# Performance work log

Hardware: AMD Instinct MI355X
Metric: run time of the kernel (lower is better)

Reference implementation:

```python
import jax, jax.numpy as jnp
import numpy as np

CON_SIZE = 1024  # num_gz; used in the 1/sqrt(con_size) score scaling


def setup_inputs() -> dict:
    key = jax.random.key(0)
    k1, k2, k3, k4, k5 = jax.random.split(key, 5)
    B, K, D, P = 1024, 256, 1024, 768
    return {
        "joint_feature": jax.random.normal(k1, (B, D), dtype=jnp.float32),
        "confounder_dictionary": jax.random.normal(k2, (K, D), dtype=jnp.float32),
        "prior": jax.random.uniform(k3, (K, 1), dtype=jnp.float32),
        "Wq": jax.random.normal(k4, (D, P), dtype=jnp.float32) * (1.0 / np.sqrt(D)),
        "Wk": jax.random.normal(k5, (D, P), dtype=jnp.float32) * (1.0 / np.sqrt(D)),
    }


def reference(joint_feature, confounder_dictionary, prior, Wq, Wk):
    # dot_product_intervention
    q = joint_feature @ Wq                       # [B, 768]
    k = confounder_dictionary @ Wk               # [K, 768]
    scores = (q @ k.T) * (1.0 / jnp.sqrt(jnp.float32(CON_SIZE)))  # [B, K]
    attn = jax.nn.softmax(scores, axis=-1)       # softmax over confounders
    # (attn[b,k,1] * conf[k,d] * prior[k,1]).sum(1)  == attn @ (conf * prior)
    g_z = jnp.einsum('bk,kd->bd', attn, confounder_dictionary * prior)  # [B, D]
    return joint_feature + g_z
```

## Files before the change

### kernel.cpp

```cpp
#include <hip/hip_runtime.h>
#include <hip/hip_bf16.h>


typedef __attribute__((ext_vector_type(8))) short short8;
typedef __attribute__((ext_vector_type(4))) float f32x4;

__device__ __forceinline__ ushort f2bf(float x) {
    union { float f; uint u; } c; c.f = x;
    return (ushort)((c.u + 0x7FFFu + ((c.u >> 16) & 1u)) >> 16);
}
__device__ __forceinline__ float bflo(uint u) {
    union { uint u; float f; } c; c.u = u << 16; return c.f;
}
__device__ __forceinline__ float bfhi(uint u) {
    union { uint u; float f; } c; c.u = u & 0xFFFF0000u; return c.f;
}

#define MFMA_BF16 __builtin_amdgcn_mfma_f32_16x16x32_bf16

__global__ __launch_bounds__(256)
void prep_kernel(const float* __restrict__ J, const float* __restrict__ conf,
                 const float* __restrict__ prior, const float* __restrict__ Wq,
                 const float* __restrict__ Wk,
                 ushort* __restrict__ Jb, ushort* __restrict__ confb,
                 ushort* __restrict__ Wqb, ushort* __restrict__ Wkb,
                 ushort* __restrict__ cpT)
{
    const int t = threadIdx.x;
    int b = blockIdx.x;

    if (b < 2816) {
        const float* src; ushort* dst; int base;
        if (b < 1024)      { src = J;    dst = Jb;    base = b * 1024; }
        else if (b < 1280) { src = conf; dst = confb; base = (b - 1024) * 1024; }
        else if (b < 2048) { src = Wq;   dst = Wqb;   base = (b - 1280) * 1024; }
        else               { src = Wk;   dst = Wkb;   base = (b - 2048) * 1024; }
        const float4 v = *(const float4*)(src + base + t * 4);
        ushort4 o;
        o.x = f2bf(v.x); o.y = f2bf(v.y); o.z = f2bf(v.z); o.w = f2bf(v.w);
        *(ushort4*)(dst + base + t * 4) = o;
        return;
    }

    __shared__ float tr[32][33];
    const int b2 = b - 2816;
    const int rt = b2 >> 5, ct = b2 & 31;
    {
        const int row = t >> 3, c4 = (t & 7) << 2;
        const float4 v = *(const float4*)(conf + (size_t)(rt * 32 + row) * 1024 + ct * 32 + c4);
        const float p = prior[rt * 32 + row];
        tr[row][c4 + 0] = v.x * p; tr[row][c4 + 1] = v.y * p;
        tr[row][c4 + 2] = v.z * p; tr[row][c4 + 3] = v.w * p;
    }
    __syncthreads();
    {
        const int orow = t >> 3, oc4 = (t & 7) << 2;
        ushort4 o;
        o.x = f2bf(tr[oc4 + 0][orow]); o.y = f2bf(tr[oc4 + 1][orow]);
        o.z = f2bf(tr[oc4 + 2][orow]); o.w = f2bf(tr[oc4 + 3][orow]);
        *(ushort4*)(cpT + (size_t)(ct * 32 + orow) * 256 + rt * 32 + oc4) = o;
    }
}

__global__ __launch_bounds__(256)
void qk_kernel(const ushort* __restrict__ Jb, const ushort* __restrict__ Wqb,
               const ushort* __restrict__ confb, const ushort* __restrict__ Wkb,
               ushort* __restrict__ qb, ushort* __restrict__ kmb)
{
    __shared__ __align__(16) ushort As[64][72];
    __shared__ __align__(16) ushort Bs[64][72];

    const int t = threadIdx.x;
    int bid = blockIdx.x;
    const ushort *A, *Wb; ushort* C;
    if (bid < 192) { A = Jb; Wb = Wqb; C = qb; }
    else           { bid -= 192; A = confb; Wb = Wkb; C = kmb; }
    const int m0 = (bid / 12) * 64, n0 = (bid % 12) * 64;

    const int wave = t >> 6, lane = t & 63;
    const int wm = (wave >> 1) * 32, wn = (wave & 1) * 32;
    const int lrow = lane & 15, quad = lane >> 4, lko = quad * 8;

    f32x4 acc[2][2];
    #pragma unroll
    for (int i = 0; i < 2; ++i)
        #pragma unroll
        for (int j = 0; j < 2; ++j) acc[i][j] = (f32x4)0.0f;

    const int sr = t >> 2, sk = (t & 3) << 4;
    const ushort* Ap = A + (size_t)(m0 + sr) * 1024 + sk;
    const int bn8 = (t & 7) * 8, bkp = t >> 3;
    const ushort* Bp = Wb + (size_t)(2 * bkp) * 768 + n0 + bn8;

    uint4 av0 = *(const uint4*)(Ap);
    uint4 av1 = *(const uint4*)(Ap + 8);
    uint4 b0  = *(const uint4*)(Bp);
    uint4 b1  = *(const uint4*)(Bp + 768);

    for (int k0 = 0; k0 < 1024; k0 += 64) {
        *(uint4*)&As[sr][sk]     = av0;
        *(uint4*)&As[sr][sk + 8] = av1;
        {
            const ushort* s0 = (const ushort*)&b0;
            const ushort* s1 = (const ushort*)&b1;
            #pragma unroll
            for (int i = 0; i < 8; ++i)
                *(uint*)&Bs[bn8 + i][2 * bkp] = (uint)s0[i] | ((uint)s1[i] << 16);
        }
        __syncthreads();
        if (k0 + 64 < 1024) {
            av0 = *(const uint4*)(Ap + k0 + 64);
            av1 = *(const uint4*)(Ap + k0 + 72);
            const ushort* Bn = Bp + (size_t)(k0 + 64) * 768;
            b0 = *(const uint4*)(Bn);
            b1 = *(const uint4*)(Bn + 768);
        }
        #pragma unroll
        for (int kk = 0; kk < 64; kk += 32) {
            const short8 a0 = *(const short8*)&As[wm + lrow][kk + lko];
            const short8 a1 = *(const short8*)&As[wm + 16 + lrow][kk + lko];
            const short8 bb0 = *(const short8*)&Bs[wn + lrow][kk + lko];
            const short8 bb1 = *(const short8*)&Bs[wn + 16 + lrow][kk + lko];
            acc[0][0] = MFMA_BF16(a0, bb0, acc[0][0], 0, 0, 0);
            acc[0][1] = MFMA_BF16(a0, bb1, acc[0][1], 0, 0, 0);
            acc[1][0] = MFMA_BF16(a1, bb0, acc[1][0], 0, 0, 0);
            acc[1][1] = MFMA_BF16(a1, bb1, acc[1][1], 0, 0, 0);
        }
        __syncthreads();
    }

    #pragma unroll
    for (int i = 0; i < 2; ++i)
        #pragma unroll
        for (int j = 0; j < 2; ++j)
            #pragma unroll
            for (int r = 0; r < 4; ++r) {
                const int m = m0 + wm + i * 16 + quad * 4 + r;
                const int n = n0 + wn + j * 16 + lrow;
                C[(size_t)m * 768 + n] = f2bf(acc[i][j][r]);
            }
}

__global__ __launch_bounds__(256)
void scores_kernel(const ushort* __restrict__ qb, const ushort* __restrict__ kmb,
                   ushort* __restrict__ sc)
{
    __shared__ __align__(16) ushort As[64][72];
    __shared__ __align__(16) ushort Bs[64][72];

    const int t = threadIdx.x;
    const int m0 = blockIdx.y * 64, n0 = blockIdx.x * 64;
    const int wave = t >> 6, lane = t & 63;
    const int wm = (wave >> 1) * 32, wn = (wave & 1) * 32;
    const int lrow = lane & 15, quad = lane >> 4, lko = quad * 8;

    f32x4 acc[2][2];
    #pragma unroll
    for (int i = 0; i < 2; ++i)
        #pragma unroll
        for (int j = 0; j < 2; ++j) acc[i][j] = (f32x4)0.0f;

    const int sr = t >> 2, sk = (t & 3) << 4;
    const ushort* Ap = qb  + (size_t)(m0 + sr) * 768 + sk;
    const ushort* Bp = kmb + (size_t)(n0 + sr) * 768 + sk;

    uint4 av0 = *(const uint4*)(Ap);
    uint4 av1 = *(const uint4*)(Ap + 8);
    uint4 bv0 = *(const uint4*)(Bp);
    uint4 bv1 = *(const uint4*)(Bp + 8);

    for (int k0 = 0; k0 < 768; k0 += 64) {
        *(uint4*)&As[sr][sk]     = av0;
        *(uint4*)&As[sr][sk + 8] = av1;
        *(uint4*)&Bs[sr][sk]     = bv0;
        *(uint4*)&Bs[sr][sk + 8] = bv1;
        __syncthreads();
        if (k0 + 64 < 768) {
            av0 = *(const uint4*)(Ap + k0 + 64);
            av1 = *(const uint4*)(Ap + k0 + 72);
            bv0 = *(const uint4*)(Bp + k0 + 64);
            bv1 = *(const uint4*)(Bp + k0 + 72);
        }
        #pragma unroll
        for (int kk = 0; kk < 64; kk += 32) {
            const short8 a0 = *(const short8*)&As[wm + lrow][kk + lko];
            const short8 a1 = *(const short8*)&As[wm + 16 + lrow][kk + lko];
            const short8 b0 = *(const short8*)&Bs[wn + lrow][kk + lko];
            const short8 b1 = *(const short8*)&Bs[wn + 16 + lrow][kk + lko];
            acc[0][0] = MFMA_BF16(a0, b0, acc[0][0], 0, 0, 0);
            acc[0][1] = MFMA_BF16(a0, b1, acc[0][1], 0, 0, 0);
            acc[1][0] = MFMA_BF16(a1, b0, acc[1][0], 0, 0, 0);
            acc[1][1] = MFMA_BF16(a1, b1, acc[1][1], 0, 0, 0);
        }
        __syncthreads();
    }

    #pragma unroll
    for (int i = 0; i < 2; ++i)
        #pragma unroll
        for (int j = 0; j < 2; ++j)
            #pragma unroll
            for (int r = 0; r < 4; ++r) {
                const int m = m0 + wm + i * 16 + quad * 4 + r;
                const int n = n0 + wn + j * 16 + lrow;
                sc[(size_t)m * 256 + n] = f2bf(acc[i][j][r] * 0.03125f);
            }
}

__global__ __launch_bounds__(256)
void out_kernel(const ushort* __restrict__ sc, const ushort* __restrict__ cpT,
                const float* __restrict__ J, float* __restrict__ out)
{
    __shared__ __align__(16) ushort At[64][264];
    __shared__ __align__(16) ushort Bs[64][72];
    __shared__ float rowInv[64];

    const int t = threadIdx.x;
    const int m0 = blockIdx.y * 64, n0 = blockIdx.x * 64;

    {
        const int row = t >> 2;
        const int cb  = (t & 3) * 64;
        const ushort* srow = sc + (size_t)(m0 + row) * 256 + cb;
        uint4 s[8];
        #pragma unroll
        for (int i = 0; i < 8; ++i) s[i] = *(const uint4*)(srow + i * 8);

        float mx = -1e30f;
        #pragma unroll
        for (int i = 0; i < 8; ++i) {
            mx = fmaxf(mx, fmaxf(fmaxf(bflo(s[i].x), bfhi(s[i].x)),
                                 fmaxf(bflo(s[i].y), bfhi(s[i].y))));
            mx = fmaxf(mx, fmaxf(fmaxf(bflo(s[i].z), bfhi(s[i].z)),
                                 fmaxf(bflo(s[i].w), bfhi(s[i].w))));
        }
        mx = fmaxf(mx, __shfl_xor(mx, 1));
        mx = fmaxf(mx, __shfl_xor(mx, 2));

        float sum = 0.0f;
        #pragma unroll
        for (int i = 0; i < 8; ++i) {
            uint4 o;
            uint* su = (uint*)&s[i];
            uint* ou = (uint*)&o;
            #pragma unroll
            for (int w = 0; w < 4; ++w) {
                const ushort e0 = f2bf(__expf(bflo(su[w]) - mx));
                const ushort e1 = f2bf(__expf(bfhi(su[w]) - mx));
                sum += bflo((uint)e0) + bflo((uint)e1);
                ou[w] = (uint)e0 | ((uint)e1 << 16);
            }
            *(uint4*)&At[row][cb + i * 8] = o;
        }
        sum += __shfl_xor(sum, 1);
        sum += __shfl_xor(sum, 2);
        if ((t & 3) == 0) rowInv[row] = 1.0f / sum;
    }
    __syncthreads();

    const int wave = t >> 6, lane = t & 63;
    const int wm = (wave >> 1) * 32, wn = (wave & 1) * 32;
    const int lrow = lane & 15, quad = lane >> 4, lko = quad * 8;

    f32x4 acc[2][2];
    #pragma unroll
    for (int i = 0; i < 2; ++i)
        #pragma unroll
        for (int j = 0; j < 2; ++j) acc[i][j] = (f32x4)0.0f;

    const int sr = t >> 2, sk = (t & 3) << 4;
    const ushort* Bp = cpT + (size_t)(n0 + sr) * 256 + sk;
    uint4 bv0 = *(const uint4*)(Bp);
    uint4 bv1 = *(const uint4*)(Bp + 8);

    for (int k0 = 0; k0 < 256; k0 += 64) {
        *(uint4*)&Bs[sr][sk]     = bv0;
        *(uint4*)&Bs[sr][sk + 8] = bv1;
        __syncthreads();
        if (k0 + 64 < 256) {
            bv0 = *(const uint4*)(Bp + k0 + 64);
            bv1 = *(const uint4*)(Bp + k0 + 72);
        }
        #pragma unroll
        for (int kk = 0; kk < 64; kk += 32) {
            const short8 a0 = *(const short8*)&At[wm + lrow][k0 + kk + lko];
            const short8 a1 = *(const short8*)&At[wm + 16 + lrow][k0 + kk + lko];
            const short8 b0 = *(const short8*)&Bs[wn + lrow][kk + lko];
            const short8 b1 = *(const short8*)&Bs[wn + 16 + lrow][kk + lko];
            acc[0][0] = MFMA_BF16(a0, b0, acc[0][0], 0, 0, 0);
            acc[0][1] = MFMA_BF16(a0, b1, acc[0][1], 0, 0, 0);
            acc[1][0] = MFMA_BF16(a1, b0, acc[1][0], 0, 0, 0);
            acc[1][1] = MFMA_BF16(a1, b1, acc[1][1], 0, 0, 0);
        }
        __syncthreads();
    }

    #pragma unroll
    for (int i = 0; i < 2; ++i)
        #pragma unroll
        for (int j = 0; j < 2; ++j)
            #pragma unroll
            for (int r = 0; r < 4; ++r) {
                const int mrel = wm + i * 16 + quad * 4 + r;
                const int m = m0 + mrel;
                const int n = n0 + wn + j * 16 + lrow;
                const size_t off = (size_t)m * 1024 + n;
                out[off] = acc[i][j][r] * rowInv[mrel] + J[off];
            }
}

extern "C" void kernel_launch(void* const* d_in, const int* in_sizes, int n_in,
                              void* d_out, int out_size, void* d_ws, size_t ws_size,
                              hipStream_t stream)
{
    const float* J     = (const float*)d_in[0];
    const float* conf  = (const float*)d_in[1];
    const float* prior = (const float*)d_in[2];
    const float* Wq    = (const float*)d_in[3];
    const float* Wk    = (const float*)d_in[4];
    float* out = (float*)d_out;

    ushort* ws = (ushort*)d_ws;
    ushort* Jb    = ws;
    ushort* confb = Jb    + 1048576;
    ushort* Wqb   = confb + 262144;
    ushort* Wkb   = Wqb   + 786432;
    ushort* cpT   = Wkb   + 786432;
    ushort* qb    = cpT   + 262144;
    ushort* kmb   = qb    + 786432;
    ushort* scb   = kmb   + 196608;

    prep_kernel<<<3072, 256, 0, stream>>>(J, conf, prior, Wq, Wk,
                                          Jb, confb, Wqb, Wkb, cpT);
    qk_kernel<<<240, 256, 0, stream>>>(Jb, Wqb, confb, Wkb, qb, kmb);
    scores_kernel<<<dim3(4, 16), 256, 0, stream>>>(qb, kmb, scb);
    out_kernel<<<dim3(16, 16), 256, 0, stream>>>(scb, cpT, J, out);
}
```

Measured before the change: 96.97 us.

## Fuse fp32-to-bf16 conversion into the Q/K projection GEMM and drop prep kernel

```diff
diff --git a/kernel.cpp b/kernel.cpp
--- a/kernel.cpp
+++ b/kernel.cpp
@@ -15,67 +15,58 @@
 __device__ __forceinline__ float bfhi(uint u) {
     union { uint u; float f; } c; c.u = u & 0xFFFF0000u; return c.f;
 }
+__device__ __forceinline__ uint fbits(float x) {
+    union { float f; uint u; } c; c.f = x; return c.u;
+}
+__device__ __forceinline__ uint pk_rhu(float lo, float hi) {
+    return ((fbits(lo) + 0x8000u) >> 16) | ((fbits(hi) + 0x8000u) & 0xFFFF0000u);
+}
 
 #define MFMA_BF16 __builtin_amdgcn_mfma_f32_16x16x32_bf16
 
+union Lds1 {
+    float tr[32][33];
+    struct {
+        __align__(16) ushort As[64][72];
+        __align__(16) ushort Bs[64][72];
+    } g;
+};
+
 __global__ __launch_bounds__(256)
-void prep_kernel(const float* __restrict__ J, const float* __restrict__ conf,
-                 const float* __restrict__ prior, const float* __restrict__ Wq,
-                 const float* __restrict__ Wk,
-                 ushort* __restrict__ Jb, ushort* __restrict__ confb,
-                 ushort* __restrict__ Wqb, ushort* __restrict__ Wkb,
-                 ushort* __restrict__ cpT)
+void l1_kernel(const float* __restrict__ J, const float* __restrict__ conf,
+               const float* __restrict__ prior, const float* __restrict__ Wq,
+               const float* __restrict__ Wk, ushort* __restrict__ qb,
+               ushort* __restrict__ kmb, ushort* __restrict__ cpT)
 {
+    __shared__ Lds1 S;
     const int t = threadIdx.x;
-    int b = blockIdx.x;
-
-    if (b < 2816) {
-        const float* src; ushort* dst; int base;
-        if (b < 1024)      { src = J;    dst = Jb;    base = b * 1024; }
-        else if (b < 1280) { src = conf; dst = confb; base = (b - 1024) * 1024; }
-        else if (b < 2048) { src = Wq;   dst = Wqb;   base = (b - 1280) * 1024; }
-        else               { src = Wk;   dst = Wkb;   base = (b - 2048) * 1024; }
-        const float4 v = *(const float4*)(src + base + t * 4);
-        ushort4 o;
-        o.x = f2bf(v.x); o.y = f2bf(v.y); o.z = f2bf(v.z); o.w = f2bf(v.w);
-        *(ushort4*)(dst + base + t * 4) = o;
+    const int bid = blockIdx.x;
+
+    if (bid >= 240) {
+        const int b2 = bid - 240;
+        const int rt = b2 >> 5, ct = b2 & 31;
+        {
+            const int row = t >> 3, c4 = (t & 7) << 2;
+            const float4 v = *(const float4*)(conf + (size_t)(rt * 32 + row) * 1024 + ct * 32 + c4);
+            const float p = prior[rt * 32 + row];
+            S.tr[row][c4 + 0] = v.x * p; S.tr[row][c4 + 1] = v.y * p;
+            S.tr[row][c4 + 2] = v.z * p; S.tr[row][c4 + 3] = v.w * p;
+        }
+        __syncthreads();
+        {
+            const int orow = t >> 3, oc4 = (t & 7) << 2;
+            ushort4 o;
+            o.x = f2bf(S.tr[oc4 + 0][orow]); o.y = f2bf(S.tr[oc4 + 1][orow]);
+            o.z = f2bf(S.tr[oc4 + 2][orow]); o.w = f2bf(S.tr[oc4 + 3][orow]);
+            *(ushort4*)(cpT + (size_t)(ct * 32 + orow) * 256 + rt * 32 + oc4) = o;
+        }
         return;
     }
 
-    __shared__ float tr[32][33];
-    const int b2 = b - 2816;
-    const int rt = b2 >> 5, ct = b2 & 31;
-    {
-        const int row = t >> 3, c4 = (t & 7) << 2;
-        const float4 v = *(const float4*)(conf + (size_t)(rt * 32 + row) * 1024 + ct * 32 + c4);
-        const float p = prior[rt * 32 + row];
-        tr[row][c4 + 0] = v.x * p; tr[row][c4 + 1] = v.y * p;
-        tr[row][c4 + 2] = v.z * p; tr[row][c4 + 3] = v.w * p;
-    }
-    __syncthreads();
-    {
-        const int orow = t >> 3, oc4 = (t & 7) << 2;
-        ushort4 o;
-        o.x = f2bf(tr[oc4 + 0][orow]); o.y = f2bf(tr[oc4 + 1][orow]);
-        o.z = f2bf(tr[oc4 + 2][orow]); o.w = f2bf(tr[oc4 + 3][orow]);
-        *(ushort4*)(cpT + (size_t)(ct * 32 + orow) * 256 + rt * 32 + oc4) = o;
-    }
-}
-
-__global__ __launch_bounds__(256)
-void qk_kernel(const ushort* __restrict__ Jb, const ushort* __restrict__ Wqb,
-               const ushort* __restrict__ confb, const ushort* __restrict__ Wkb,
-               ushort* __restrict__ qb, ushort* __restrict__ kmb)
-{
-    __shared__ __align__(16) ushort As[64][72];
-    __shared__ __align__(16) ushort Bs[64][72];
-
-    const int t = threadIdx.x;
-    int bid = blockIdx.x;
-    const ushort *A, *Wb; ushort* C;
-    if (bid < 192) { A = Jb; Wb = Wqb; C = qb; }
-    else           { bid -= 192; A = confb; Wb = Wkb; C = kmb; }
-    const int m0 = (bid / 12) * 64, n0 = (bid % 12) * 64;
+    const float *A, *Bm; ushort* C; int m0, n0;
+    if (bid < 192) { A = J;    Bm = Wq; C = qb;  m0 = (bid / 12) * 64; n0 = (bid % 12) * 64; }
+    else { const int b2 = bid - 192;
+           A = conf; Bm = Wk; C = kmb; m0 = (b2  / 12) * 64; n0 = (b2  % 12) * 64; }
 
     const int wave = t >> 6, lane = t & 63;
     const int wm = (wave >> 1) * 32, wn = (wave & 1) * 32;
@@ -87,44 +78,60 @@
         #pragma unroll
         for (int j = 0; j < 2; ++j) acc[i][j] = (f32x4)0.0f;
 
-    const int sr = t >> 2, sk = (t & 3) << 4;
-    const ushort* Ap = A + (size_t)(m0 + sr) * 1024 + sk;
-    const int bn8 = (t & 7) * 8, bkp = t >> 3;
-    const ushort* Bp = Wb + (size_t)(2 * bkp) * 768 + n0 + bn8;
-
-    uint4 av0 = *(const uint4*)(Ap);
-    uint4 av1 = *(const uint4*)(Ap + 8);
-    uint4 b0  = *(const uint4*)(Bp);
-    uint4 b1  = *(const uint4*)(Bp + 768);
+    const int sr = t >> 2, q4 = (t & 3) << 4;
+    const int bn = (t & 15) << 2, bk = (t >> 4) << 1;
+    const float* Ap = A + (size_t)(m0 + sr) * 1024 + q4;
+    const float* Bp = Bm + (size_t)bk * 768 + n0 + bn;
+
+    float4 aF0 = *(const float4*)(Ap + 0),  aF1 = *(const float4*)(Ap + 4);
+    float4 aF2 = *(const float4*)(Ap + 8),  aF3 = *(const float4*)(Ap + 12);
+    float4 bF0 = *(const float4*)(Bp);
+    float4 bF1 = *(const float4*)(Bp + 768);
+    float4 bF2 = *(const float4*)(Bp + (size_t)32 * 768);
+    float4 bF3 = *(const float4*)(Bp + (size_t)33 * 768);
 
     for (int k0 = 0; k0 < 1024; k0 += 64) {
-        *(uint4*)&As[sr][sk]     = av0;
-        *(uint4*)&As[sr][sk + 8] = av1;
         {
-            const ushort* s0 = (const ushort*)&b0;
-            const ushort* s1 = (const ushort*)&b1;
-            #pragma unroll
-            for (int i = 0; i < 8; ++i)
-                *(uint*)&Bs[bn8 + i][2 * bkp] = (uint)s0[i] | ((uint)s1[i] << 16);
+            uint2 w;
+            w.x = pk_rhu(aF0.x, aF0.y); w.y = pk_rhu(aF0.z, aF0.w);
+            *(uint2*)&S.g.As[sr][q4 + 0] = w;
+            w.x = pk_rhu(aF1.x, aF1.y); w.y = pk_rhu(aF1.z, aF1.w);
+            *(uint2*)&S.g.As[sr][q4 + 4] = w;
+            w.x = pk_rhu(aF2.x, aF2.y); w.y = pk_rhu(aF2.z, aF2.w);
+            *(uint2*)&S.g.As[sr][q4 + 8] = w;
+            w.x = pk_rhu(aF3.x, aF3.y); w.y = pk_rhu(aF3.z, aF3.w);
+            *(uint2*)&S.g.As[sr][q4 + 12] = w;
+            *(uint*)&S.g.Bs[bn + 0][bk]      = pk_rhu(bF0.x, bF1.x);
+            *(uint*)&S.g.Bs[bn + 1][bk]      = pk_rhu(bF0.y, bF1.y);
+            *(uint*)&S.g.Bs[bn + 2][bk]      = pk_rhu(bF0.z, bF1.z);
+            *(uint*)&S.g.Bs[bn + 3][bk]      = pk_rhu(bF0.w, bF1.w);
+            *(uint*)&S.g.Bs[bn + 0][bk + 32] = pk_rhu(bF2.x, bF3.x);
+            *(uint*)&S.g.Bs[bn + 1][bk + 32] = pk_rhu(bF2.y, bF3.y);
+            *(uint*)&S.g.Bs[bn + 2][bk + 32] = pk_rhu(bF2.z, bF3.z);
+            *(uint*)&S.g.Bs[bn + 3][bk + 32] = pk_rhu(bF2.w, bF3.w);
         }
         __syncthreads();
         if (k0 + 64 < 1024) {
-            av0 = *(const uint4*)(Ap + k0 + 64);
-            av1 = *(const uint4*)(Ap + k0 + 72);
-            const ushort* Bn = Bp + (size_t)(k0 + 64) * 768;
-            b0 = *(const uint4*)(Bn);
-            b1 = *(const uint4*)(Bn + 768);
+            aF0 = *(const float4*)(Ap + k0 + 64);
+            aF1 = *(const float4*)(Ap + k0 + 68);
+            aF2 = *(const float4*)(Ap + k0 + 72);
+            aF3 = *(const float4*)(Ap + k0 + 76);
+            const float* Bn = Bp + (size_t)(k0 + 64) * 768;
+            bF0 = *(const float4*)(Bn);
+            bF1 = *(const float4*)(Bn + 768);
+            bF2 = *(const float4*)(Bn + (size_t)32 * 768);
+            bF3 = *(const float4*)(Bn + (size_t)33 * 768);
         }
         #pragma unroll
         for (int kk = 0; kk < 64; kk += 32) {
-            const short8 a0 = *(const short8*)&As[wm + lrow][kk + lko];
-            const short8 a1 = *(const short8*)&As[wm + 16 + lrow][kk + lko];
-            const short8 bb0 = *(const short8*)&Bs[wn + lrow][kk + lko];
-            const short8 bb1 = *(const short8*)&Bs[wn + 16 + lrow][kk + lko];
-            acc[0][0] = MFMA_BF16(a0, bb0, acc[0][0], 0, 0, 0);
-            acc[0][1] = MFMA_BF16(a0, bb1, acc[0][1], 0, 0, 0);
-            acc[1][0] = MFMA_BF16(a1, bb0, acc[1][0], 0, 0, 0);
-            acc[1][1] = MFMA_BF16(a1, bb1, acc[1][1], 0, 0, 0);
+            const short8 a0 = *(const short8*)&S.g.As[wm + lrow][kk + lko];
+            const short8 a1 = *(const short8*)&S.g.As[wm + 16 + lrow][kk + lko];
+            const short8 b0 = *(const short8*)&S.g.Bs[wn + lrow][kk + lko];
+            const short8 b1 = *(const short8*)&S.g.Bs[wn + 16 + lrow][kk + lko];
+            acc[0][0] = MFMA_BF16(a0, b0, acc[0][0], 0, 0, 0);
+            acc[0][1] = MFMA_BF16(a0, b1, acc[0][1], 0, 0, 0);
+            acc[1][0] = MFMA_BF16(a1, b0, acc[1][0], 0, 0, 0);
+            acc[1][1] = MFMA_BF16(a1, b1, acc[1][1], 0, 0, 0);
         }
         __syncthreads();
     }
@@ -320,19 +327,13 @@
     const float* Wk    = (const float*)d_in[4];
     float* out = (float*)d_out;
 
-    ushort* ws = (ushort*)d_ws;
-    ushort* Jb    = ws;
-    ushort* confb = Jb    + 1048576;
-    ushort* Wqb   = confb + 262144;
-    ushort* Wkb   = Wqb   + 786432;
-    ushort* cpT   = Wkb   + 786432;
-    ushort* qb    = cpT   + 262144;
-    ushort* kmb   = qb    + 786432;
-    ushort* scb   = kmb   + 196608;
-
-    prep_kernel<<<3072, 256, 0, stream>>>(J, conf, prior, Wq, Wk,
-                                          Jb, confb, Wqb, Wkb, cpT);
-    qk_kernel<<<240, 256, 0, stream>>>(Jb, Wqb, confb, Wkb, qb, kmb);
+    ushort* ws  = (ushort*)d_ws;
+    ushort* qb  = ws;
+    ushort* kmb = qb  + 786432;
+    ushort* cpT = kmb + 196608;
+    ushort* scb = cpT + 262144;
+
+    l1_kernel<<<496, 256, 0, stream>>>(J, conf, prior, Wq, Wk, qb, kmb, cpT);
     scores_kernel<<<dim3(4, 16), 256, 0, stream>>>(qb, kmb, scb);
     out_kernel<<<dim3(16, 16), 256, 0, stream>>>(scb, cpT, J, out);
 }
```

Result: no change. 98.21 us (+1.3%).
